# Kernel tuning notes

Measured on AMD Instinct MI355X. Metric: run time of the kernel, lower is better.

## Reference

```python
import jax, jax.numpy as jnp
import numpy as np

EPS = 1e-5
J = 17


def build_adj(num_joints=J):
    edges = [(0, 1), (1, 2), (1, 3), (3, 4), (4, 5), (1, 6), (6, 7), (7, 8),
             (0, 9), (9, 10), (10, 11), (0, 12), (12, 13), (13, 14)]
    if num_joints > 15:
        edges.extend([(11, 15), (14, 16)])
    adj = np.eye(num_joints, dtype=np.float32)
    for i, j in edges:
        if i < num_joints and j < num_joints:
            adj[i, j] = 1.0
            adj[j, i] = 1.0
    adj = adj / adj.sum(axis=1, keepdims=True)
    return jnp.asarray(adj)


def _bn(x, g, b, m, v):
    # inference-mode BatchNorm2d over channel axis 1 of (B,C,T,J)
    scale = (g / jnp.sqrt(v + EPS))[None, :, None, None]
    shift = (b - m * g / jnp.sqrt(v + EPS))[None, :, None, None]
    return x * scale + shift


def _conv1x1(x, w, b):
    # x: (B,C,T,J), w: (O,C) -> (B,O,T,J)
    return jnp.einsum('oc,bctj->botj', w, x) + b[None, :, None, None]


def _tconv(x, w, b):
    # temporal conv kernel (3,1), padding (1,0); x: (B,C,T,J), w: (O,C,3)
    y = jax.lax.conv_general_dilated(
        x, w[:, :, :, None], window_strides=(1, 1),
        padding=[(1, 1), (0, 0)],
        dimension_numbers=('NCHW', 'OIHW', 'NCHW'))
    return y + b[None, :, None, None]


def _block(x, adj, sw, sb, sg, sbb, sm, sv, tw, tb, tg, tbb, tm, tv,
           rw, rb, rg, rbb, rm, rv):
    residual = _bn(_conv1x1(x, rw, rb), rg, rbb, rm, rv)
    y = jnp.einsum('bctj,jk->bctk', x, adj)
    y = jax.nn.relu(_bn(_conv1x1(y, sw, sb), sg, sbb, sm, sv))
    y = _bn(_tconv(y, tw, tb), tg, tbb, tm, tv)
    return jax.nn.relu(y + residual)  # dropout is identity in eval mode


def setup_inputs() -> dict:
    key = jax.random.key(0)
    ks = iter(jax.random.split(key, 64))
    B, T = 16, 2048

    def randn(shape, s=0.1):
        return jax.random.normal(next(ks), shape, dtype=jnp.float32) * s

    def bn_params(c):
        g = 1.0 + randn((c,), 0.05)
        b = randn((c,), 0.05)
        m = randn((c,), 0.1)
        v = jax.random.uniform(next(ks), (c,), minval=0.5, maxval=1.5)
        return g, b, m, v

    inp = {
        'x': jax.random.normal(next(ks), (B, 3, T, J), dtype=jnp.float32),
        'adj': build_adj(J),
    }
    # block 0: 3 -> 64
    inp['b0_sw'] = randn((64, 3)); inp['b0_sb'] = randn((64,), 0.02)
    inp['b0_sg'], inp['b0_sbb'], inp['b0_sm'], inp['b0_sv'] = bn_params(64)
    inp['b0_tw'] = randn((64, 64, 3), 0.05); inp['b0_tb'] = randn((64,), 0.02)
    inp['b0_tg'], inp['b0_tbb'], inp['b0_tm'], inp['b0_tv'] = bn_params(64)
    inp['b0_rw'] = randn((64, 3)); inp['b0_rb'] = randn((64,), 0.02)
    inp['b0_rg'], inp['b0_rbb'], inp['b0_rm'], inp['b0_rv'] = bn_params(64)
    # block 1: 64 -> 128
    inp['b1_sw'] = randn((128, 64), 0.05); inp['b1_sb'] = randn((128,), 0.02)
    inp['b1_sg'], inp['b1_sbb'], inp['b1_sm'], inp['b1_sv'] = bn_params(128)
    inp['b1_tw'] = randn((128, 128, 3), 0.03); inp['b1_tb'] = randn((128,), 0.02)
    inp['b1_tg'], inp['b1_tbb'], inp['b1_tm'], inp['b1_tv'] = bn_params(128)
    inp['b1_rw'] = randn((128, 64), 0.05); inp['b1_rb'] = randn((128,), 0.02)
    inp['b1_rg'], inp['b1_rbb'], inp['b1_rm'], inp['b1_rv'] = bn_params(128)
    # projection 128 -> 128
    inp['proj_w'] = randn((128, 128), 0.05); inp['proj_b'] = randn((128,), 0.02)
    return inp


def reference(x, adj,
              b0_sw, b0_sb, b0_sg, b0_sbb, b0_sm, b0_sv,
              b0_tw, b0_tb, b0_tg, b0_tbb, b0_tm, b0_tv,
              b0_rw, b0_rb, b0_rg, b0_rbb, b0_rm, b0_rv,
              b1_sw, b1_sb, b1_sg, b1_sbb, b1_sm, b1_sv,
              b1_tw, b1_tb, b1_tg, b1_tbb, b1_tm, b1_tv,
              b1_rw, b1_rb, b1_rg, b1_rbb, b1_rm, b1_rv,
              proj_w, proj_b):
    y = _block(x, adj, b0_sw, b0_sb, b0_sg, b0_sbb, b0_sm, b0_sv,
               b0_tw, b0_tb, b0_tg, b0_tbb, b0_tm, b0_tv,
               b0_rw, b0_rb, b0_rg, b0_rbb, b0_rm, b0_rv)
    y = _block(y, adj, b1_sw, b1_sb, b1_sg, b1_sbb, b1_sm, b1_sv,
               b1_tw, b1_tb, b1_tg, b1_tbb, b1_tm, b1_tv,
               b1_rw, b1_rb, b1_rg, b1_rbb, b1_rm, b1_rv)
    y = y.mean(axis=-1)            # (B, C, T)
    y = y.transpose(0, 2, 1)       # (B, T, C)
    return jnp.einsum('btc,ec->bte', y, proj_w) + proj_b  # (B, T, embed)
```

## Files before the change

### kernel.cpp

```cpp
#include <hip/hip_runtime.h>
#include <hip/hip_bf16.h>
#include <stdint.h>

typedef __attribute__((ext_vector_type(8))) short bf16x8;
typedef __attribute__((ext_vector_type(4))) float f32x4;

#define EPSB 1e-5f

#define W0TE_B   0u
#define W1SB_B   24576u
#define W1E_B    40960u
#define W1R_B    139264u
#define PROJW_B  155648u
#define WS0F_B   188416u
#define WR0F_B   189440u
#define BS0F_B   190464u
#define CB0F_B   190720u
#define BS1F_B   190976u
#define CB1F_B   191488u
#define SPT_B    192000u
#define SCRATCH_B 193536u
#define Y0_PERB  4456448ull

__device__ __forceinline__ float bf2f(unsigned int u16v) {
    union { unsigned int i; float f; } v; v.i = u16v << 16; return v.f;
}
__device__ __forceinline__ unsigned short f2bf(float f) {
    unsigned int x = __float_as_uint(f);
    x = x + 0x7fffu + ((x >> 16) & 1u);
    return (unsigned short)(x >> 16);
}
__device__ __forceinline__ unsigned pk2(float a, float b) {
    union { __hip_bfloat162 h; unsigned u; } v;
    v.h = __float22bfloat162_rn(make_float2(a, b));
    return v.u;
}
__device__ __forceinline__ int div17(int p) { return (p * 241) >> 12; }

struct PrepArgs {
    const float *sw0,*sb0,*sg0,*sbb0,*sm0,*sv0;
    const float *tw0,*tb0,*tg0,*tbb0,*tm0,*tv0;
    const float *rw0,*rb0,*rg0,*rbb0,*rm0,*rv0;
    const float *sw1,*sb1,*sg1,*sbb1,*sm1,*sv1;
    const float *tw1,*tb1,*tg1,*tbb1,*tm1,*tv1;
    const float *rw1,*rb1,*rg1,*rbb1,*rm1,*rv1;
    const float *projw;
    const float *adj;
    unsigned char* ws;
};

__global__ void prep_kernel(PrepArgs a) {
    const int g = blockIdx.x * 256 + threadIdx.x;
    unsigned short* W0TE  = (unsigned short*)(a.ws + W0TE_B);
    unsigned short* W1SBp = (unsigned short*)(a.ws + W1SB_B);
    unsigned short* W1Ep  = (unsigned short*)(a.ws + W1E_B);
    unsigned short* W1Rp  = (unsigned short*)(a.ws + W1R_B);
    unsigned short* PROJW = (unsigned short*)(a.ws + PROJW_B);
    float* WS0F = (float*)(a.ws + WS0F_B);
    float* WR0F = (float*)(a.ws + WR0F_B);
    float* BS0F = (float*)(a.ws + BS0F_B);
    float* CB0F = (float*)(a.ws + CB0F_B);
    float* BS1F = (float*)(a.ws + BS1F_B);
    float* CB1F = (float*)(a.ws + CB1F_B);
    float2* SPT = (float2*)(a.ws + SPT_B);

    if (g < 64) {
        int o = g;
        float scs = a.sg0[o] / sqrtf(a.sv0[o] + EPSB);
        BS0F[o] = scs * (a.sb0[o] - a.sm0[o]) + a.sbb0[o];
        for (int c = 0; c < 4; c++) WS0F[o*4+c] = (c < 3) ? scs * a.sw0[o*3+c] : 0.f;
        float tct = a.tg0[o] / sqrtf(a.tv0[o] + EPSB);
        float rcr = a.rg0[o] / sqrtf(a.rv0[o] + EPSB);
        CB0F[o] = tct * (a.tb0[o] - a.tm0[o]) + a.tbb0[o]
                + rcr * (a.rb0[o] - a.rm0[o]) + a.rbb0[o];
        for (int c = 0; c < 4; c++) WR0F[o*4+c] = (c < 3) ? rcr * a.rw0[o*3+c] : 0.f;
    } else if (g < 192) {
        int o = g - 64;
        float scs = a.sg1[o] / sqrtf(a.sv1[o] + EPSB);
        BS1F[o] = scs * (a.sb1[o] - a.sm1[o]) + a.sbb1[o];
        float tct = a.tg1[o] / sqrtf(a.tv1[o] + EPSB);
        float rcr = a.rg1[o] / sqrtf(a.rv1[o] + EPSB);
        CB1F[o] = tct * (a.tb1[o] - a.tm1[o]) + a.tbb1[o]
                + rcr * (a.rb1[o] - a.rm1[o]) + a.rbb1[o];
    } else if (g < 12480) {
        int idx = g - 192;
        int o = idx / 192, k = idx % 192, tap = k >> 6, c = k & 63;
        float tct = a.tg0[o] / sqrtf(a.tv0[o] + EPSB);
        W0TE[o*192 + k] = f2bf(tct * a.tw0[(o*64 + c)*3 + tap]);
    } else if (g < 20672) {
        int idx = g - 12480;
        int o = idx >> 6, c = idx & 63;
        float scs = a.sg1[o] / sqrtf(a.sv1[o] + EPSB);
        W1SBp[o*64 + c] = f2bf(scs * a.sw1[o*64 + c]);
    } else if (g < 69824) {
        int idx = g - 20672;
        int h = idx / 24576, r = idx % 24576;
        int o = r / 192, k = r % 192, tap = k >> 6, c = (h << 6) + (k & 63);
        float tct = a.tg1[o] / sqrtf(a.tv1[o] + EPSB);
        W1Ep[(h*128 + o)*192 + k] = f2bf(tct * a.tw1[(o*128 + c)*3 + tap]);
    } else if (g < 78016) {
        int idx = g - 69824;
        int o = idx >> 6, c = idx & 63;
        float rcr = a.rg1[o] / sqrtf(a.rv1[o] + EPSB);
        W1Rp[o*64 + c] = f2bf(rcr * a.rw1[o*64 + c]);
    } else if (g < 94400) {
        int idx = g - 78016;
        PROJW[idx] = f2bf(a.projw[idx]);
    } else if (g < 94417) {
        int j = g - 94400;
        int cnt = 0;
        for (int k = 0; k < 17; k++) {
            float v = a.adj[k*17 + j];
            if (v != 0.0f && cnt < 8) {
                SPT[j*8 + cnt] = make_float2(v, __uint_as_float((unsigned)k));
                cnt++;
            }
        }
        for (; cnt < 8; cnt++) SPT[j*8 + cnt] = make_float2(0.f, __uint_as_float(0u));
    }
}

__launch_bounds__(256, 3)
__global__ void b0_kernel(const float* __restrict__ x,
                          const unsigned char* __restrict__ ws,
                          unsigned short* __restrict__ Y0,
                          unsigned short* __restrict__ YG, int b0base) {
    __shared__ float xt[510];
    __shared__ float xg[510];
    __shared__ float2 sptA[136];
    __shared__ float2 sptB[136];
    __shared__ float Ws0s[256], Wr0s[256], bs0s[64], cb0s[64];
    __shared__ __align__(16) unsigned short s0[170*72];
    __shared__ __align__(16) unsigned short yst[136*72];

    const int tid = threadIdx.x;
    const int b_loc = blockIdx.x >> 8;
    const int b = b0base + b_loc;
    const int t0 = (blockIdx.x & 255) << 3;
    const int Pb = (t0 - 1) * 17;

    const int w = tid >> 6, l = tid & 63, lr = l & 15, lg = l >> 4;
    const int n = w*16 + lr;

    const unsigned short* W0TE = (const unsigned short*)(ws + W0TE_B);
    bf16x8 bfr[6];
    #pragma unroll
    for (int ks = 0; ks < 6; ks++)
        bfr[ks] = *(const bf16x8*)&W0TE[n*192 + ks*32 + lg*8];

    if (tid < 136) {
        float2 raw = ((const float2*)(ws + SPT_B))[tid];
        sptA[tid] = make_float2(raw.x, __uint_as_float(__float_as_uint(raw.y) * 4u));
        sptB[tid] = make_float2(raw.x, __uint_as_float(__float_as_uint(raw.y) * 144u));
    }
    Ws0s[tid] = ((const float*)(ws + WS0F_B))[tid];
    Wr0s[tid] = ((const float*)(ws + WR0F_B))[tid];
    if (tid < 64) {
        bs0s[tid] = ((const float*)(ws + BS0F_B))[tid];
        cb0s[tid] = ((const float*)(ws + CB0F_B))[tid];
    }
    #pragma unroll
    for (int it = 0; it < 2; it++) {
        int idx = tid + it*256;
        if (idx < 510) {
            int c = idx / 170, r = idx - c*170;
            int P = Pb + r;
            float v = 0.f;
            if (P >= 0 && P < 34816) v = x[(size_t)(b*3 + c)*34816 + P];
            xt[idx] = v;
        }
    }
    __syncthreads();
    #pragma unroll
    for (int it = 0; it < 2; it++) {
        int idx = tid + it*256;
        if (idx < 510) {
            int c = idx / 170, r = idx - c*170;
            int j = r - 17*div17(r);
            const char* rowb = (const char*)&xt[c*170 + (r - j)];
            float acc = 0.f;
            #pragma unroll
            for (int i = 0; i < 8; i++) {
                float2 e = sptA[j*8 + i];
                acc += e.x * *(const float*)(rowb + __float_as_uint(e.y));
            }
            xg[idx] = acc;
        }
    }
    __syncthreads();
    #pragma unroll
    for (int it = 0; it < 11; it++) {
        int idx = tid + it*256;
        if (idx < 2720) {
            int r = idx >> 4, cg = idx & 15, o0 = cg*4;
            int P = Pb + r;
            uint2 pkv = make_uint2(0u, 0u);
            if (P >= 0 && P < 34816) {
                float a0 = xg[r], a1 = xg[170 + r], a2 = xg[340 + r];
                float v0 = fmaxf(bs0s[o0]   + Ws0s[(o0  )*4]*a0 + Ws0s[(o0  )*4+1]*a1 + Ws0s[(o0  )*4+2]*a2, 0.f);
                float v1 = fmaxf(bs0s[o0+1] + Ws0s[(o0+1)*4]*a0 + Ws0s[(o0+1)*4+1]*a1 + Ws0s[(o0+1)*4+2]*a2, 0.f);
                float v2 = fmaxf(bs0s[o0+2] + Ws0s[(o0+2)*4]*a0 + Ws0s[(o0+2)*4+1]*a1 + Ws0s[(o0+2)*4+2]*a2, 0.f);
                float v3 = fmaxf(bs0s[o0+3] + Ws0s[(o0+3)*4]*a0 + Ws0s[(o0+3)*4+1]*a1 + Ws0s[(o0+3)*4+2]*a2, 0.f);
                pkv.x = pk2(v0, v1); pkv.y = pk2(v2, v3);
            }
            *(uint2*)&s0[r*72 + o0] = pkv;
        }
    }
    __syncthreads();
    {
        const float wr0 = Wr0s[n*4], wr1 = Wr0s[n*4+1], wr2 = Wr0s[n*4+2];
        const float cbn = cb0s[n];
        for (int mb = 0; mb < 9; mb++) {
            const int ra = mb*16 + lr;
            f32x4 acc = {0.f, 0.f, 0.f, 0.f};
            #pragma unroll
            for (int ks = 0; ks < 6; ks++) {
                int row = ra + (ks >> 1)*17; if (row > 169) row = 169;
                const int c0 = ((ks & 1) << 5) + lg*8;
                acc = __builtin_amdgcn_mfma_f32_16x16x32_bf16(
                    *(const bf16x8*)&s0[row*72 + c0], bfr[ks], acc, 0, 0, 0);
            }
            const int mbase = mb*16 + lg*4;
            #pragma unroll
            for (int i = 0; i < 4; i++) {
                const int m = mbase + i;
                if (m < 136) {
                    float v = acc[i] + cbn + wr0*xt[m+17] + wr1*xt[170+m+17] + wr2*xt[340+m+17];
                    yst[m*72 + n] = f2bf(fmaxf(v, 0.f));
                }
            }
        }
    }
    __syncthreads();
    #pragma unroll
    for (int it = 0; it < 5; it++) {
        int idx = tid + it*256;
        if (idx < 1088) {
            int m = idx >> 3, seg = idx & 7;
            uint4 v = *(const uint4*)&yst[m*72 + seg*8];
            *(uint4*)&Y0[((size_t)b_loc*34816 + t0*17 + m)*64 + seg*8] = v;
        }
    }
    #pragma unroll
    for (int it = 0; it < 9; it++) {
        int idx = tid + it*256;
        if (idx < 2176) {
            int p = idx >> 4, cg = idx & 15;
            int j = p - 17*div17(p);
            const char* rowb = (const char*)yst + (p - j)*144 + cg*8;
            float a0=0.f, a1=0.f, a2=0.f, a3=0.f;
            #pragma unroll
            for (int i = 0; i < 8; i++) {
                float2 e = sptB[j*8 + i];
                uint2 u = *(const uint2*)(rowb + __float_as_uint(e.y));
                a0 += e.x * __uint_as_float(u.x << 16);
                a1 += e.x * __uint_as_float(u.x & 0xffff0000u);
                a2 += e.x * __uint_as_float(u.y << 16);
                a3 += e.x * __uint_as_float(u.y & 0xffff0000u);
            }
            uint2 o; o.x = pk2(a0, a1); o.y = pk2(a2, a3);
            *(uint2*)&YG[((size_t)b_loc*34816 + t0*17 + p)*64 + cg*4] = o;
        }
    }
}

__launch_bounds__(512, 2)
__global__ void b1_kernel(const unsigned char* __restrict__ ws,
                          const unsigned short* __restrict__ Y0,
                          const unsigned short* __restrict__ YG,
                          const float* __restrict__ projb,
                          float* __restrict__ outp, int b0base) {
    __shared__ __align__(16) unsigned short smem[36720];
    __shared__ __align__(16) unsigned short meansP[16*136];
    __shared__ float cb1s[128], bs1s[128];

    unsigned short* ybuf  = smem;
    unsigned short* ygbuf = smem + 12240;
    unsigned short* s0buf = smem + 24480;

    const int tid = threadIdx.x;
    const int b_loc = blockIdx.x >> 6;
    const int ck = blockIdx.x & 63;
    const int gb = b0base + b_loc;

    const unsigned short* W1SBp = (const unsigned short*)(ws + W1SB_B);
    const unsigned short* W1Ep  = (const unsigned short*)(ws + W1E_B);
    const unsigned short* W1Rp  = (const unsigned short*)(ws + W1R_B);
    const unsigned short* PROJW = (const unsigned short*)(ws + PROJW_B);

    const int w = tid >> 6, l = tid & 63, lr = l & 15, lg = l >> 4;
    const int n = w*16 + lr;
    const int sNt = w & 3, sMh = w >> 2;
    const int nloc_s = sNt*16 + lr;

    if (tid < 128) {
        cb1s[tid] = ((const float*)(ws + CB1F_B))[tid];
        bs1s[tid] = ((const float*)(ws + BS1F_B))[tid];
    }
    bf16x8 rb0 = *(const bf16x8*)&W1Rp[n*64 + lg*8];
    bf16x8 rb1 = *(const bf16x8*)&W1Rp[n*64 + 32 + lg*8];

    uint4 pf[5];
    auto PF = [&](int t0n) {
        const int Pbn = t0n*17 - 17;
        #pragma unroll
        for (int s = 0; s < 5; s++) {
            int idx = tid + s*512;
            uint4 v = make_uint4(0u,0u,0u,0u);
            if (idx < 1360) {
                int p = idx >> 3, seg = idx & 7;
                int P = Pbn + p;
                if (P >= 0 && P < 34816)
                    v = *(const uint4*)&YG[((size_t)b_loc*34816 + P)*64 + seg*8];
            } else if (idx < 2448) {
                int p = (idx - 1360) >> 3, seg = (idx - 1360) & 7;
                v = *(const uint4*)&Y0[((size_t)b_loc*34816 + t0n*17 + p)*64 + seg*8];
            }
            pf[s] = v;
        }
    };
    PF(ck << 5);

    for (int tt = 0; tt < 4; tt++) {
        const int t0 = (ck << 5) + (tt << 3);
        const int Pb = (t0 - 1) * 17;
        const bool edge = (Pb < 0) || (Pb + 169 >= 34816);

        #pragma unroll
        for (int s = 0; s < 5; s++) {
            int idx = tid + s*512;
            if (idx < 1360) {
                int p = idx >> 3, seg = idx & 7;
                *(uint4*)&ygbuf[p*72 + seg*8] = pf[s];
            } else if (idx < 2448) {
                int p = (idx - 1360) >> 3, seg = (idx - 1360) & 7;
                *(uint4*)&ybuf[(17 + p)*72 + seg*8] = pf[s];
            }
        }
        __syncthreads();

        if (tt < 3) PF(t0 + 8);

        f32x4 tacc[9];
        #pragma unroll
        for (int mb = 0; mb < 9; mb++) {
            const int row = 17 + mb*16 + lr;
            f32x4 acc = {0.f, 0.f, 0.f, 0.f};
            acc = __builtin_amdgcn_mfma_f32_16x16x32_bf16(*(const bf16x8*)&ybuf[row*72 + lg*8],      rb0, acc, 0, 0, 0);
            acc = __builtin_amdgcn_mfma_f32_16x16x32_bf16(*(const bf16x8*)&ybuf[row*72 + 32 + lg*8], rb1, acc, 0, 0, 0);
            tacc[mb] = acc;
        }
        {
            bf16x8 sbA = *(const bf16x8*)&W1SBp[(nloc_s)*64 + lg*8];
            bf16x8 sbB = *(const bf16x8*)&W1SBp[(nloc_s)*64 + 32 + lg*8];
            const float bias = bs1s[nloc_s];
            const int mbS = sMh ? 6 : 0, mbE = sMh ? 11 : 6;
            if (!edge) {
                for (int mb = mbS; mb < mbE; mb++) {
                    int ra = mb*16 + lr; if (ra > 169) ra = 169;
                    f32x4 sa = {0.f, 0.f, 0.f, 0.f};
                    sa = __builtin_amdgcn_mfma_f32_16x16x32_bf16(*(const bf16x8*)&ygbuf[ra*72 + lg*8],      sbA, sa, 0, 0, 0);
                    sa = __builtin_amdgcn_mfma_f32_16x16x32_bf16(*(const bf16x8*)&ygbuf[ra*72 + 32 + lg*8], sbB, sa, 0, 0, 0);
                    const int mbase = mb*16 + lg*4;
                    #pragma unroll
                    for (int i = 0; i < 4; i++) {
                        int m = mbase + i;
                        if (m < 170) s0buf[m*72 + nloc_s] = f2bf(fmaxf(sa[i] + bias, 0.f));
                    }
                }
            } else {
                for (int mb = mbS; mb < mbE; mb++) {
                    int ra = mb*16 + lr; if (ra > 169) ra = 169;
                    f32x4 sa = {0.f, 0.f, 0.f, 0.f};
                    sa = __builtin_amdgcn_mfma_f32_16x16x32_bf16(*(const bf16x8*)&ygbuf[ra*72 + lg*8],      sbA, sa, 0, 0, 0);
                    sa = __builtin_amdgcn_mfma_f32_16x16x32_bf16(*(const bf16x8*)&ygbuf[ra*72 + 32 + lg*8], sbB, sa, 0, 0, 0);
                    const int mbase = mb*16 + lg*4;
                    #pragma unroll
                    for (int i = 0; i < 4; i++) {
                        int m = mbase + i;
                        if (m < 170) {
                            int P = Pb + m;
                            float v = (P >= 0 && P < 34816) ? fmaxf(sa[i] + bias, 0.f) : 0.f;
                            s0buf[m*72 + nloc_s] = f2bf(v);
                        }
                    }
                }
            }
        }
        __syncthreads();

        {
            bf16x8 bfh[6];
            #pragma unroll
            for (int ks = 0; ks < 6; ks++)
                bfh[ks] = *(const bf16x8*)&W1Ep[n*192 + ks*32 + lg*8];
            __builtin_amdgcn_s_setprio(1);
            #pragma unroll
            for (int mb = 0; mb < 9; mb++) {
                const int ma = mb*16 + lr;
                f32x4 acc = tacc[mb];
                #pragma unroll
                for (int ks = 0; ks < 6; ks++) {
                    int row = ma + (ks >> 1)*17; if (row > 169) row = 169;
                    const int c0 = ((ks & 1) << 5) + lg*8;
                    acc = __builtin_amdgcn_mfma_f32_16x16x32_bf16(
                        *(const bf16x8*)&s0buf[row*72 + c0], bfh[ks], acc, 0, 0, 0);
                }
                tacc[mb] = acc;
            }
            __builtin_amdgcn_s_setprio(0);
        }
        {
            bf16x8 sbA = *(const bf16x8*)&W1SBp[(64 + nloc_s)*64 + lg*8];
            bf16x8 sbB = *(const bf16x8*)&W1SBp[(64 + nloc_s)*64 + 32 + lg*8];
            const float bias = bs1s[64 + nloc_s];
            const int mbS = sMh ? 6 : 0, mbE = sMh ? 11 : 6;
            if (!edge) {
                for (int mb = mbS; mb < mbE; mb++) {
                    int ra = mb*16 + lr; if (ra > 169) ra = 169;
                    f32x4 sa = {0.f, 0.f, 0.f, 0.f};
                    sa = __builtin_amdgcn_mfma_f32_16x16x32_bf16(*(const bf16x8*)&ygbuf[ra*72 + lg*8],      sbA, sa, 0, 0, 0);
                    sa = __builtin_amdgcn_mfma_f32_16x16x32_bf16(*(const bf16x8*)&ygbuf[ra*72 + 32 + lg*8], sbB, sa, 0, 0, 0);
                    const int mbase = mb*16 + lg*4;
                    #pragma unroll
                    for (int i = 0; i < 4; i++) {
                        int m = mbase + i;
                        if (m < 170) ybuf[m*72 + nloc_s] = f2bf(fmaxf(sa[i] + bias, 0.f));
                    }
                }
            } else {
                for (int mb = mbS; mb < mbE; mb++) {
                    int ra = mb*16 + lr; if (ra > 169) ra = 169;
                    f32x4 sa = {0.f, 0.f, 0.f, 0.f};
                    sa = __builtin_amdgcn_mfma_f32_16x16x32_bf16(*(const bf16x8*)&ygbuf[ra*72 + lg*8],      sbA, sa, 0, 0, 0);
                    sa = __builtin_amdgcn_mfma_f32_16x16x32_bf16(*(const bf16x8*)&ygbuf[ra*72 + 32 + lg*8], sbB, sa, 0, 0, 0);
                    const int mbase = mb*16 + lg*4;
                    #pragma unroll
                    for (int i = 0; i < 4; i++) {
                        int m = mbase + i;
                        if (m < 170) {
                            int P = Pb + m;
                            float v = (P >= 0 && P < 34816) ? fmaxf(sa[i] + bias, 0.f) : 0.f;
                            ybuf[m*72 + nloc_s] = f2bf(v);
                        }
                    }
                }
            }
        }
        __syncthreads();

        {
            bf16x8 bfh[6];
            #pragma unroll
            for (int ks = 0; ks < 6; ks++)
                bfh[ks] = *(const bf16x8*)&W1Ep[(128 + n)*192 + ks*32 + lg*8];
            __builtin_amdgcn_s_setprio(1);
            #pragma unroll
            for (int mb = 0; mb < 9; mb++) {
                const int ma = mb*16 + lr;
                f32x4 acc = tacc[mb];
                #pragma unroll
                for (int ks = 0; ks < 6; ks++) {
                    int row = ma + (ks >> 1)*17; if (row > 169) row = 169;
                    const int c0 = ((ks & 1) << 5) + lg*8;
                    acc = __builtin_amdgcn_mfma_f32_16x16x32_bf16(
                        *(const bf16x8*)&ybuf[row*72 + c0], bfh[ks], acc, 0, 0, 0);
                }
                tacc[mb] = acc;
            }
            __builtin_amdgcn_s_setprio(0);
        }
        {
            const float cb = cb1s[n];
            float mv0 = 0.f, mv1 = 0.f;
            #pragma unroll
            for (int t = 0; t < 8; t++) {
                float s = 0.f;
                #pragma unroll
                for (int mb = 0; mb < 9; mb++) {
                    #pragma unroll
                    for (int i = 0; i < 4; i++) {
                        const int mlo = mb*16 + i;
                        if (mlo + 12 >= t*17 && mlo <= t*17 + 16 && mlo < 136) {
                            int m = mlo + lg*4;
                            bool in = (m >= t*17) && (m <= t*17 + 16) && (m < 136);
                            float v = fmaxf(tacc[mb][i] + cb, 0.f);
                            s += in ? v : 0.f;
                        }
                    }
                }
                s += __shfl_xor(s, 16, 64);
                s += __shfl_xor(s, 32, 64);
                float mval = s * (1.f / 17.f);
                if (t == lg)     mv0 = mval;
                if (t == lg + 4) mv1 = mval;
            }
            const int mrow = (tt & 1) * 8;
            meansP[(mrow + lg)*136 + n]     = f2bf(mv0);
            meansP[(mrow + 4 + lg)*136 + n] = f2bf(mv1);
        }
        __syncthreads();

        if (tt & 1) {
            const int et = w;
            bf16x8 pw[4];
            #pragma unroll
            for (int kf = 0; kf < 4; kf++)
                pw[kf] = *(const bf16x8*)&PROJW[(et*16 + lr)*128 + kf*32 + lg*8];
            f32x4 pa = {0.f, 0.f, 0.f, 0.f};
            #pragma unroll
            for (int kf = 0; kf < 4; kf++)
                pa = __builtin_amdgcn_mfma_f32_16x16x32_bf16(
                    *(const bf16x8*)&meansP[lr*136 + kf*32 + lg*8], pw[kf], pa, 0, 0, 0);
            const float pb = projb[et*16 + lr];
            const int tbase = ck*32 + (tt - 1)*8;
            #pragma unroll
            for (int i = 0; i < 4; i++) {
                const int m = lg*4 + i;
                outp[((size_t)gb*2048 + tbase + m)*128 + et*16 + lr] = pa[i] + pb;
            }
        }
    }
}

extern "C" void kernel_launch(void* const* d_in, const int* in_sizes, int n_in,
                              void* d_out, int out_size, void* d_ws, size_t ws_size,
                              hipStream_t stream) {
    const float* x     = (const float*)d_in[0];
    const float* adj   = (const float*)d_in[1];
    const float* projb = (const float*)d_in[39];
    unsigned char* ws  = (unsigned char*)d_ws;

    PrepArgs pa;
    pa.sw0 = (const float*)d_in[2];  pa.sb0  = (const float*)d_in[3];
    pa.sg0 = (const float*)d_in[4];  pa.sbb0 = (const float*)d_in[5];
    pa.sm0 = (const float*)d_in[6];  pa.sv0  = (const float*)d_in[7];
    pa.tw0 = (const float*)d_in[8];  pa.tb0  = (const float*)d_in[9];
    pa.tg0 = (const float*)d_in[10]; pa.tbb0 = (const float*)d_in[11];
    pa.tm0 = (const float*)d_in[12]; pa.tv0  = (const float*)d_in[13];
    pa.rw0 = (const float*)d_in[14]; pa.rb0  = (const float*)d_in[15];
    pa.rg0 = (const float*)d_in[16]; pa.rbb0 = (const float*)d_in[17];
    pa.rm0 = (const float*)d_in[18]; pa.rv0  = (const float*)d_in[19];
    pa.sw1 = (const float*)d_in[20]; pa.sb1  = (const float*)d_in[21];
    pa.sg1 = (const float*)d_in[22]; pa.sbb1 = (const float*)d_in[23];
    pa.sm1 = (const float*)d_in[24]; pa.sv1  = (const float*)d_in[25];
    pa.tw1 = (const float*)d_in[26]; pa.tb1  = (const float*)d_in[27];
    pa.tm1 = (const float*)d_in[30]; pa.tbb1 = (const float*)d_in[29];
    pa.tg1 = (const float*)d_in[28];
    pa.tv1  = (const float*)d_in[31];
    pa.rw1 = (const float*)d_in[32]; pa.rb1  = (const float*)d_in[33];
    pa.rg1 = (const float*)d_in[34]; pa.rbb1 = (const float*)d_in[35];
    pa.rm1 = (const float*)d_in[36]; pa.rv1  = (const float*)d_in[37];
    pa.projw = (const float*)d_in[38];
    pa.adj = adj;
    pa.ws = ws;

    prep_kernel<<<dim3(369), dim3(256), 0, stream>>>(pa);

    const size_t perb = 2ull * Y0_PERB;
    int chunk = 16;
    while (chunk > 1 && (size_t)SCRATCH_B + (size_t)chunk * perb > ws_size) chunk >>= 1;

    unsigned short* Y0p = (unsigned short*)(ws + SCRATCH_B);
    unsigned short* YGp = (unsigned short*)((unsigned char*)Y0p + (size_t)chunk * Y0_PERB);

    for (int cb = 0; cb < 16; cb += chunk) {
        b0_kernel<<<dim3(chunk * 256), dim3(256), 0, stream>>>(x, ws, Y0p, YGp, cb);
        b1_kernel<<<dim3(chunk * 64), dim3(512), 0, stream>>>(ws, Y0p, YGp, projb, (float*)d_out, cb);
    }
}
```

Before: 353.0 us.

## Retile block-1 GEMMs so each wave owns a 3x4 MFMA tile over time-joint rows

```diff
diff --git a/kernel.cpp b/kernel.cpp
--- a/kernel.cpp
+++ b/kernel.cpp
@@ -289,7 +289,8 @@
     const unsigned short* PROJW = (const unsigned short*)(ws + PROJW_B);
 
     const int w = tid >> 6, l = tid & 63, lr = l & 15, lg = l >> 4;
-    const int n = w*16 + lr;
+    const int wM = w & 3, wN = w >> 2;
+    const int rM = wM * 34;
     const int sNt = w & 3, sMh = w >> 2;
     const int nloc_s = sNt*16 + lr;
 
@@ -297,8 +298,6 @@
         cb1s[tid] = ((const float*)(ws + CB1F_B))[tid];
         bs1s[tid] = ((const float*)(ws + BS1F_B))[tid];
     }
-    bf16x8 rb0 = *(const bf16x8*)&W1Rp[n*64 + lg*8];
-    bf16x8 rb1 = *(const bf16x8*)&W1Rp[n*64 + 32 + lg*8];
 
     uint4 pf[5];
     auto PF = [&](int t0n) {
@@ -341,14 +340,30 @@
 
         if (tt < 3) PF(t0 + 8);
 
-        f32x4 tacc[9];
+        f32x4 tacc[3][4];
         #pragma unroll
-        for (int mb = 0; mb < 9; mb++) {
-            const int row = 17 + mb*16 + lr;
-            f32x4 acc = {0.f, 0.f, 0.f, 0.f};
-            acc = __builtin_amdgcn_mfma_f32_16x16x32_bf16(*(const bf16x8*)&ybuf[row*72 + lg*8],      rb0, acc, 0, 0, 0);
-            acc = __builtin_amdgcn_mfma_f32_16x16x32_bf16(*(const bf16x8*)&ybuf[row*72 + 32 + lg*8], rb1, acc, 0, 0, 0);
-            tacc[mb] = acc;
+        for (int mbL = 0; mbL < 3; mbL++)
+            #pragma unroll
+            for (int nb = 0; nb < 4; nb++) tacc[mbL][nb] = (f32x4){0.f,0.f,0.f,0.f};
+
+        {
+            bf16x8 ra_[3][2];
+            #pragma unroll
+            for (int mbL = 0; mbL < 3; mbL++)
+                #pragma unroll
+                for (int kf = 0; kf < 2; kf++)
+                    ra_[mbL][kf] = *(const bf16x8*)&ybuf[(17 + rM + mbL*16 + lr)*72 + kf*32 + lg*8];
+            #pragma unroll
+            for (int nb = 0; nb < 4; nb++) {
+                const int n = wN*64 + nb*16 + lr;
+                bf16x8 rb0 = *(const bf16x8*)&W1Rp[n*64 + lg*8];
+                bf16x8 rb1 = *(const bf16x8*)&W1Rp[n*64 + 32 + lg*8];
+                #pragma unroll
+                for (int mbL = 0; mbL < 3; mbL++) {
+                    tacc[mbL][nb] = __builtin_amdgcn_mfma_f32_16x16x32_bf16(ra_[mbL][0], rb0, tacc[mbL][nb], 0, 0, 0);
+                    tacc[mbL][nb] = __builtin_amdgcn_mfma_f32_16x16x32_bf16(ra_[mbL][1], rb1, tacc[mbL][nb], 0, 0, 0);
+                }
+            }
         }
         {
             bf16x8 sbA = *(const bf16x8*)&W1SBp[(nloc_s)*64 + lg*8];
@@ -390,23 +405,27 @@
         __syncthreads();
 
         {
-            bf16x8 bfh[6];
-            #pragma unroll
-            for (int ks = 0; ks < 6; ks++)
-                bfh[ks] = *(const bf16x8*)&W1Ep[n*192 + ks*32 + lg*8];
+            bf16x8 af[3][6];
+            #pragma unroll
+            for (int mbL = 0; mbL < 3; mbL++)
+                #pragma unroll
+                for (int ks = 0; ks < 6; ks++) {
+                    int row = rM + mbL*16 + lr + (ks >> 1)*17; if (row > 169) row = 169;
+                    af[mbL][ks] = *(const bf16x8*)&s0buf[row*72 + ((ks & 1) << 5) + lg*8];
+                }
             __builtin_amdgcn_s_setprio(1);
             #pragma unroll
-            for (int mb = 0; mb < 9; mb++) {
-                const int ma = mb*16 + lr;
-                f32x4 acc = tacc[mb];
-                #pragma unroll
-                for (int ks = 0; ks < 6; ks++) {
-                    int row = ma + (ks >> 1)*17; if (row > 169) row = 169;
-                    const int c0 = ((ks & 1) << 5) + lg*8;
-                    acc = __builtin_amdgcn_mfma_f32_16x16x32_bf16(
-                        *(const bf16x8*)&s0buf[row*72 + c0], bfh[ks], acc, 0, 0, 0);
-                }
-                tacc[mb] = acc;
+            for (int nb = 0; nb < 4; nb++) {
+                const int n = wN*64 + nb*16 + lr;
+                bf16x8 bf_[6];
+                #pragma unroll
+                for (int ks = 0; ks < 6; ks++)
+                    bf_[ks] = *(const bf16x8*)&W1Ep[n*192 + ks*32 + lg*8];
+                #pragma unroll
+                for (int mbL = 0; mbL < 3; mbL++)
+                    #pragma unroll
+                    for (int ks = 0; ks < 6; ks++)
+                        tacc[mbL][nb] = __builtin_amdgcn_mfma_f32_16x16x32_bf16(af[mbL][ks], bf_[ks], tacc[mbL][nb], 0, 0, 0);
             }
             __builtin_amdgcn_s_setprio(0);
         }
@@ -450,54 +469,59 @@
         __syncthreads();
 
         {
-            bf16x8 bfh[6];
-            #pragma unroll
-            for (int ks = 0; ks < 6; ks++)
-                bfh[ks] = *(const bf16x8*)&W1Ep[(128 + n)*192 + ks*32 + lg*8];
+            bf16x8 af[3][6];
+            #pragma unroll
+            for (int mbL = 0; mbL < 3; mbL++)
+                #pragma unroll
+                for (int ks = 0; ks < 6; ks++) {
+                    int row = rM + mbL*16 + lr + (ks >> 1)*17; if (row > 169) row = 169;
+                    af[mbL][ks] = *(const bf16x8*)&ybuf[row*72 + ((ks & 1) << 5) + lg*8];
+                }
             __builtin_amdgcn_s_setprio(1);
             #pragma unroll
-            for (int mb = 0; mb < 9; mb++) {
-                const int ma = mb*16 + lr;
-                f32x4 acc = tacc[mb];
-                #pragma unroll
-                for (int ks = 0; ks < 6; ks++) {
-                    int row = ma + (ks >> 1)*17; if (row > 169) row = 169;
-                    const int c0 = ((ks & 1) << 5) + lg*8;
-                    acc = __builtin_amdgcn_mfma_f32_16x16x32_bf16(
-                        *(const bf16x8*)&ybuf[row*72 + c0], bfh[ks], acc, 0, 0, 0);
-                }
-                tacc[mb] = acc;
+            for (int nb = 0; nb < 4; nb++) {
+                const int n = wN*64 + nb*16 + lr;
+                bf16x8 bf_[6];
+                #pragma unroll
+                for (int ks = 0; ks < 6; ks++)
+                    bf_[ks] = *(const bf16x8*)&W1Ep[(128 + n)*192 + ks*32 + lg*8];
+                #pragma unroll
+                for (int mbL = 0; mbL < 3; mbL++)
+                    #pragma unroll
+                    for (int ks = 0; ks < 6; ks++)
+                        tacc[mbL][nb] = __builtin_amdgcn_mfma_f32_16x16x32_bf16(af[mbL][ks], bf_[ks], tacc[mbL][nb], 0, 0, 0);
             }
             __builtin_amdgcn_s_setprio(0);
         }
         {
-            const float cb = cb1s[n];
-            float mv0 = 0.f, mv1 = 0.f;
-            #pragma unroll
-            for (int t = 0; t < 8; t++) {
-                float s = 0.f;
-                #pragma unroll
-                for (int mb = 0; mb < 9; mb++) {
-                    #pragma unroll
-                    for (int i = 0; i < 4; i++) {
-                        const int mlo = mb*16 + i;
-                        if (mlo + 12 >= t*17 && mlo <= t*17 + 16 && mlo < 136) {
-                            int m = mlo + lg*4;
-                            bool in = (m >= t*17) && (m <= t*17 + 16) && (m < 136);
-                            float v = fmaxf(tacc[mb][i] + cb, 0.f);
-                            s += in ? v : 0.f;
-                        }
-                    }
-                }
-                s += __shfl_xor(s, 16, 64);
-                s += __shfl_xor(s, 32, 64);
-                float mval = s * (1.f / 17.f);
-                if (t == lg)     mv0 = mval;
-                if (t == lg + 4) mv1 = mval;
-            }
-            const int mrow = (tt & 1) * 8;
-            meansP[(mrow + lg)*136 + n]     = f2bf(mv0);
-            meansP[(mrow + 4 + lg)*136 + n] = f2bf(mv1);
+            const int nbase = wN*64 + lr;
+            const int mrow = (tt & 1) * 8 + wM*2;
+            #pragma unroll
+            for (int nb = 0; nb < 4; nb++) {
+                const float cbv = cb1s[nbase + nb*16];
+                float v00 = fmaxf(tacc[0][nb][0] + cbv, 0.f);
+                float v01 = fmaxf(tacc[0][nb][1] + cbv, 0.f);
+                float v02 = fmaxf(tacc[0][nb][2] + cbv, 0.f);
+                float v03 = fmaxf(tacc[0][nb][3] + cbv, 0.f);
+                float v10 = fmaxf(tacc[1][nb][0] + cbv, 0.f);
+                float v11 = fmaxf(tacc[1][nb][1] + cbv, 0.f);
+                float v12 = fmaxf(tacc[1][nb][2] + cbv, 0.f);
+                float v13 = fmaxf(tacc[1][nb][3] + cbv, 0.f);
+                float v20 = fmaxf(tacc[2][nb][0] + cbv, 0.f);
+                float v21 = fmaxf(tacc[2][nb][1] + cbv, 0.f);
+                float s0 = v00 + v01 + v02 + v03;
+                float s1v = v10 + v11 + v12 + v13;
+                float bnd  = (lg == 0) ? v10 : 0.f;
+                float tail = (lg == 0) ? (v20 + v21) : 0.f;
+                float t0s = s0 + bnd;
+                float t1s = s1v - bnd + tail;
+                t0s += __shfl_xor(t0s, 16, 64); t0s += __shfl_xor(t0s, 32, 64);
+                t1s += __shfl_xor(t1s, 16, 64); t1s += __shfl_xor(t1s, 32, 64);
+                if (lg == nb) {
+                    meansP[(mrow    )*136 + nbase + nb*16] = f2bf(t0s * (1.f/17.f));
+                    meansP[(mrow + 1)*136 + nbase + nb*16] = f2bf(t1s * (1.f/17.f));
+                }
+            }
         }
         __syncthreads();
 
@@ -545,9 +569,8 @@
     pa.sg1 = (const float*)d_in[22]; pa.sbb1 = (const float*)d_in[23];
     pa.sm1 = (const float*)d_in[24]; pa.sv1  = (const float*)d_in[25];
     pa.tw1 = (const float*)d_in[26]; pa.tb1  = (const float*)d_in[27];
-    pa.tm1 = (const float*)d_in[30]; pa.tbb1 = (const float*)d_in[29];
-    pa.tg1 = (const float*)d_in[28];
-    pa.tv1  = (const float*)d_in[31];
+    pa.tg1 = (const float*)d_in[28]; pa.tbb1 = (const float*)d_in[29];
+    pa.tm1 = (const float*)d_in[30]; pa.tv1  = (const float*)d_in[31];
     pa.rw1 = (const float*)d_in[32]; pa.rb1  = (const float*)d_in[33];
     pa.rg1 = (const float*)d_in[34]; pa.rbb1 = (const float*)d_in[35];
     pa.rm1 = (const float*)d_in[36]; pa.rv1  = (const float*)d_in[37];
```

Result: slower. 674.1 us (+91.0%).
